# Performance work log

Measured on AMD Instinct MI355X. Metric: run time of the kernel, lower is better.

The kernel has to match this reference:

```python
import jax, jax.numpy as jnp
import numpy as np

B, S, H, D = 4, 2048, 16, 64


def setup_inputs() -> dict:
    key = jax.random.key(0)
    kq, kk, kv, kl = jax.random.split(key, 4)
    qs = jax.random.normal(kq, (B, S, H, D), dtype=jnp.float32)
    ks = jax.random.normal(kk, (B, S, H, D), dtype=jnp.float32)
    vs = jax.random.normal(kv, (B, S, H, D), dtype=jnp.float32)
    # valid lengths in [S//2, S] so no sequence is fully masked out
    valid_lens = jax.random.randint(kl, (B,), S // 2, S + 1, dtype=jnp.int32)
    return {"qs": qs, "ks": ks, "vs": vs, "valid_lens": valid_lens}


def reference(qs, ks, vs, valid_lens):
    # ScanAttention == exact softmax attention (FlashAttention-2 is an
    # IO-aware reformulation of the same math). qs scaled by 1/sqrt(D).
    d = qs.shape[-1]
    scale = 1.0 / jnp.sqrt(jnp.asarray(d, qs.dtype))
    # scores: [B, H, Q, K]
    scores = jnp.einsum('bqhd,bkhd->bhqk', qs * scale, ks)
    # key mask from valid_lens: position k is valid iff k < valid_lens[b]
    k_len = ks.shape[1]
    ks_mask = jnp.arange(k_len)[None, :] < valid_lens[:, None]  # [B, K]
    scores = jnp.where(ks_mask[:, None, None, :], scores, -jnp.inf)
    attn = jax.nn.softmax(scores, axis=-1)
    ctx = jnp.einsum('bhqk,bkhd->bqhd', attn, vs)
    return ctx
```

## Files before the change

### kernel.cpp

```cpp
#include <hip/hip_runtime.h>
#include <hip/hip_bf16.h>

typedef __bf16 bf16x8 __attribute__((ext_vector_type(8)));
typedef float  f32x4  __attribute__((ext_vector_type(4)));
typedef float  f32x16 __attribute__((ext_vector_type(16)));
typedef float  f4     __attribute__((ext_vector_type(4)));
typedef unsigned int u32;
typedef u32 u32x4 __attribute__((ext_vector_type(4)));

#define MFMA16(a,b,c) __builtin_amdgcn_mfma_f32_16x16x32_bf16(a,b,c,0,0,0)
#define MFMA32(a,b,c) __builtin_amdgcn_mfma_f32_32x32x16_bf16(a,b,c,0,0,0)

constexpr int   Bc = 4, Sc = 2048, Hc = 16, Dc = 64;
constexpr int   HD  = Hc * Dc;
constexpr int   SHD = Sc * HD;
constexpr float SCALE = 0.125f;
constexpr float LOG2E = 1.4426950408889634f;
constexpr float QSC   = SCALE * LOG2E;
constexpr float NEG   = -1e30f;
constexpr int   HEAD_ELEMS = Sc * Dc;
constexpr size_t KV_ELEMS  = (size_t)Bc * Hc * HEAD_ELEMS;

__global__ __launch_bounds__(256) void prep2(
    const float* __restrict__ K, const float* __restrict__ V,
    __bf16* __restrict__ Kf, __bf16* __restrict__ Vf)
{
    __shared__ __align__(16) __bf16 KT[64][80];
    __shared__ __align__(16) __bf16 VT[64][80];

    const int bid = blockIdx.x;
    const int st  = bid & 31;
    const int h   = (bid >> 5) & 15;
    const int b   = bid >> 9;
    const int tid = threadIdx.x;
    const int sl  = tid >> 2;
    const int d0  = (tid & 3) * 16;
    const size_t iof = ((size_t)(b * 2048 + st * 64 + sl) * 16 + h) * 64 + d0;

    #pragma unroll
    for (int q = 0; q < 2; ++q) {
        f4 a = __builtin_nontemporal_load((const f4*)(K + iof + q * 8));
        f4 c = __builtin_nontemporal_load((const f4*)(K + iof + q * 8 + 4));
        bf16x8 w;
        w[0]=(__bf16)a.x; w[1]=(__bf16)a.y; w[2]=(__bf16)a.z; w[3]=(__bf16)a.w;
        w[4]=(__bf16)c.x; w[5]=(__bf16)c.y; w[6]=(__bf16)c.z; w[7]=(__bf16)c.w;
        *(bf16x8*)&KT[sl][d0 + q * 8] = w;
    }
    #pragma unroll
    for (int q = 0; q < 2; ++q) {
        f4 a = __builtin_nontemporal_load((const f4*)(V + iof + q * 8));
        f4 c = __builtin_nontemporal_load((const f4*)(V + iof + q * 8 + 4));
        bf16x8 w;
        w[0]=(__bf16)a.x; w[1]=(__bf16)a.y; w[2]=(__bf16)a.z; w[3]=(__bf16)a.w;
        w[4]=(__bf16)c.x; w[5]=(__bf16)c.y; w[6]=(__bf16)c.z; w[7]=(__bf16)c.w;
        *(bf16x8*)&VT[sl][d0 + q * 8] = w;
    }
    __syncthreads();

    const size_t hbase = (size_t)(b * 16 + h) * HEAD_ELEMS;

    #pragma unroll
    for (int it = 0; it < 2; ++it) {
        const int idx = it * 256 + tid;
        const int tl  = idx >> 8;
        const int dk  = (idx >> 6) & 3;
        const int ln  = idx & 63;
        const int l31 = ln & 31, lhi = ln >> 5;
        bf16x8 w = *(const bf16x8*)&KT[tl * 32 + l31][dk * 16 + lhi * 8];
        *(bf16x8*)(Kf + hbase + (size_t)(((st * 2 + tl) * 4 + dk) * 512 + ln * 8)) = w;
    }
    #pragma unroll
    for (int it = 0; it < 2; ++it) {
        const int idx  = it * 256 + tid;
        const int tl   = idx >> 8;
        const int dblk = (idx >> 7) & 1;
        const int kt2  = (idx >> 6) & 1;
        const int ln   = idx & 63;
        const int l31  = ln & 31, lhi = ln >> 5;
        bf16x8 w;
        #pragma unroll
        for (int j = 0; j < 8; ++j)
            w[j] = VT[tl * 32 + kt2 * 16 + lhi * 8 + j][dblk * 32 + l31];
        *(bf16x8*)(Vf + hbase +
            (size_t)(((((st * 2 + tl) * 2 + dblk) * 2 + kt2)) * 512 + ln * 8)) = w;
    }
}

__global__ __launch_bounds__(64, 4) void fattn4(
    const float* __restrict__ Q, const __bf16* __restrict__ Kf,
    const __bf16* __restrict__ Vf, const int* __restrict__ VL,
    float* __restrict__ O)
{
    const int bid  = blockIdx.x;
    const int l    = (bid & 7) * 512 + (bid >> 3);
    const int head = l >> 6;
    const int qt   = l & 63;
    const int b    = head >> 4;
    const int h    = head & 15;
    const int lane = threadIdx.x;
    const int l31  = lane & 31;
    const int hi   = lane >> 5;
    const int vl   = VL[b];

    const size_t qbase = (size_t)b * SHD + (size_t)h * Dc;
    const __bf16* kfh = Kf + (size_t)head * HEAD_ELEMS + lane * 8;
    const __bf16* vfh = Vf + (size_t)head * HEAD_ELEMS + lane * 8;
    const int qrow0 = qt * 32;

    bf16x8 qf[4];
    {
        const float* qp = Q + qbase + (size_t)(qrow0 + l31) * HD + hi * 8;
        #pragma unroll
        for (int dk = 0; dk < 4; ++dk) {
            f4 x0 = __builtin_nontemporal_load((const f4*)(qp + dk * 16));
            f4 x1 = __builtin_nontemporal_load((const f4*)(qp + dk * 16 + 4));
            bf16x8 f;
            f[0]=(__bf16)(x0.x*QSC); f[1]=(__bf16)(x0.y*QSC);
            f[2]=(__bf16)(x0.z*QSC); f[3]=(__bf16)(x0.w*QSC);
            f[4]=(__bf16)(x1.x*QSC); f[5]=(__bf16)(x1.y*QSC);
            f[6]=(__bf16)(x1.z*QSC); f[7]=(__bf16)(x1.w*QSC);
            qf[dk] = f;
        }
    }

    f32x16 acc0, acc1;
    #pragma unroll
    for (int i = 0; i < 16; ++i) { acc0[i] = 0.f; acc1[i] = 0.f; }
    float m = NEG, lsum = 0.f;

    const int nt   = (vl + 31) >> 5;
    const int ntm1 = nt - 1;
    const bool hastail = (vl & 31) != 0;

    bf16x8 kf[4], vf[4];
    #pragma unroll
    for (int dk = 0; dk < 4; ++dk) kf[dk] = *(const bf16x8*)(kfh + dk * 512);
    #pragma unroll
    for (int i = 0; i < 4; ++i)   vf[i]  = *(const bf16x8*)(vfh + i * 512);

    for (int t = 0; t < nt; ++t) {
        f32x16 s;
        #pragma unroll
        for (int i = 0; i < 16; ++i) s[i] = 0.f;
        #pragma unroll
        for (int dk = 0; dk < 4; ++dk) s = MFMA32(kf[dk], qf[dk], s);

        {
            const size_t off = (size_t)((t < ntm1) ? t + 1 : t) * 2048;
            #pragma unroll
            for (int dk = 0; dk < 4; ++dk)
                kf[dk] = *(const bf16x8*)(kfh + off + dk * 512);
        }

        if (t == ntm1 && hastail) {
            const int kv0 = t * 32;
            #pragma unroll
            for (int i = 0; i < 16; ++i) {
                const int key = kv0 + (i & 3) + 8 * (i >> 2) + 4 * hi;
                if (key >= vl) s[i] = NEG;
            }
        }

        float a0 = fmaxf(s[0], s[1]),  a1 = fmaxf(s[2], s[3]);
        float a2 = fmaxf(s[4], s[5]),  a3 = fmaxf(s[6], s[7]);
        float a4 = fmaxf(s[8], s[9]),  a5 = fmaxf(s[10], s[11]);
        float a6 = fmaxf(s[12], s[13]), a7 = fmaxf(s[14], s[15]);
        float b0 = fmaxf(a0, a1), b1 = fmaxf(a2, a3);
        float b2 = fmaxf(a4, a5), b3 = fmaxf(a6, a7);
        float tm = fmaxf(fmaxf(b0, b1), fmaxf(b2, b3));
        tm = fmaxf(tm, __shfl_xor(tm, 32));

        if (__any(tm > m + 8.0f)) {
            const float mn  = fmaxf(m, tm);
            const float fac = __builtin_amdgcn_exp2f(m - mn);
            lsum *= fac;
            #pragma unroll
            for (int i = 0; i < 16; ++i) { acc0[i] *= fac; acc1[i] *= fac; }
            m = mn;
        }
        #pragma unroll
        for (int i = 0; i < 16; ++i)
            s[i] = __builtin_amdgcn_exp2f(s[i] - m);
        {
            float t0 = (s[0]+s[1]) + (s[2]+s[3]);
            float t1 = (s[4]+s[5]) + (s[6]+s[7]);
            float t2 = (s[8]+s[9]) + (s[10]+s[11]);
            float t3 = (s[12]+s[13]) + (s[14]+s[15]);
            lsum += (t0 + t1) + (t2 + t3);
        }

        bf16x8 ap[2];
        #pragma unroll
        for (int kt = 0; kt < 2; ++kt) {
            u32 w0, w1, w2, w3;
            asm("v_cvt_pk_bf16_f32 %0, %1, %2" : "=v"(w0) : "v"(s[8*kt+0]), "v"(s[8*kt+1]));
            asm("v_cvt_pk_bf16_f32 %0, %1, %2" : "=v"(w1) : "v"(s[8*kt+2]), "v"(s[8*kt+3]));
            asm("v_cvt_pk_bf16_f32 %0, %1, %2" : "=v"(w2) : "v"(s[8*kt+4]), "v"(s[8*kt+5]));
            asm("v_cvt_pk_bf16_f32 %0, %1, %2" : "=v"(w3) : "v"(s[8*kt+6]), "v"(s[8*kt+7]));
            const u32 sx0 = (u32)__shfl_xor((int)w0, 32);
            const u32 sx1 = (u32)__shfl_xor((int)w1, 32);
            const u32 sx2 = (u32)__shfl_xor((int)w2, 32);
            const u32 sx3 = (u32)__shfl_xor((int)w3, 32);
            u32x4 fw;
            fw.x = hi ? sx2 : w0;
            fw.y = hi ? sx3 : w1;
            fw.z = hi ? w2 : sx0;
            fw.w = hi ? w3 : sx1;
            ap[kt] = __builtin_bit_cast(bf16x8, fw);
        }

        acc0 = MFMA32(vf[0], ap[0], acc0);
        acc0 = MFMA32(vf[1], ap[1], acc0);
        acc1 = MFMA32(vf[2], ap[0], acc1);
        acc1 = MFMA32(vf[3], ap[1], acc1);

        {
            const size_t off = (size_t)((t < ntm1) ? t + 1 : t) * 2048;
            #pragma unroll
            for (int i = 0; i < 4; ++i)
                vf[i] = *(const bf16x8*)(vfh + off + i * 512);
        }
    }

    const float lfull = lsum + __shfl_xor(lsum, 32);
    const float linv  = 1.0f / lfull;
    float* op = O + qbase + (size_t)(qrow0 + l31) * HD;
    #pragma unroll
    for (int qd = 0; qd < 4; ++qd) {
        f4 w0, w1;
        w0.x = acc0[4*qd+0]*linv; w0.y = acc0[4*qd+1]*linv;
        w0.z = acc0[4*qd+2]*linv; w0.w = acc0[4*qd+3]*linv;
        w1.x = acc1[4*qd+0]*linv; w1.y = acc1[4*qd+1]*linv;
        w1.z = acc1[4*qd+2]*linv; w1.w = acc1[4*qd+3]*linv;
        __builtin_nontemporal_store(w0, (f4*)(op + qd * 8 + 4 * hi));
        __builtin_nontemporal_store(w1, (f4*)(op + 32 + qd * 8 + 4 * hi));
    }
}

__global__ __launch_bounds__(256, 2) void fattn_fb(
    const float* __restrict__ Q, const float* __restrict__ K,
    const float* __restrict__ V, const int* __restrict__ VL,
    float* __restrict__ O)
{
    __shared__ __bf16 Vts[64 * 64];
    __shared__ __bf16 Pl[4][32 * 64];
    const int bid = blockIdx.x;
    const int qt = bid & 15, h = (bid >> 4) & 15, b = bid >> 8;
    const int tid = threadIdx.x, wid = tid >> 6, lane = tid & 63;
    const int li = lane & 15, lg = lane >> 4;
    const int vl = VL[b];
    const size_t base = (size_t)b * SHD + (size_t)h * Dc;
    bf16x8 aq[2][2];
    const int qrow0 = qt * 128 + wid * 32;
    #pragma unroll
    for (int m = 0; m < 2; ++m) {
        const float* qp = Q + base + (size_t)(qrow0 + m * 16 + li) * HD + lg * 8;
        #pragma unroll
        for (int ks = 0; ks < 2; ++ks) {
            float4 x0 = *(const float4*)(qp + ks * 32);
            float4 x1 = *(const float4*)(qp + ks * 32 + 4);
            bf16x8 f;
            f[0]=(__bf16)(x0.x*QSC); f[1]=(__bf16)(x0.y*QSC);
            f[2]=(__bf16)(x0.z*QSC); f[3]=(__bf16)(x0.w*QSC);
            f[4]=(__bf16)(x1.x*QSC); f[5]=(__bf16)(x1.y*QSC);
            f[6]=(__bf16)(x1.z*QSC); f[7]=(__bf16)(x1.w*QSC);
            aq[m][ks] = f;
        }
    }
    bf16x8 bones;
    #pragma unroll
    for (int j = 0; j < 8; ++j) bones[j] = (__bf16)1.0f;
    f32x4 acc[2][4]; float mst[2][4], lst[2][4];
    #pragma unroll
    for (int m = 0; m < 2; ++m) {
        #pragma unroll
        for (int r = 0; r < 4; ++r) { mst[m][r] = NEG; lst[m][r] = 0.f; }
        #pragma unroll
        for (int dt = 0; dt < 4; ++dt)
            #pragma unroll
            for (int r = 0; r < 4; ++r) acc[m][dt][r] = 0.f;
    }
    const int ntiles = (vl + 63) >> 6;
    const int sd = tid & 63, skb = (tid >> 6) * 8;
    const float* vpd = V + base + sd;
    for (int t = 0; t < ntiles; ++t) {
        const int kv0 = t * 64;
        __syncthreads();
        #pragma unroll
        for (int rep = 0; rep < 2; ++rep) {
            const int kb2 = skb + rep * 32;
            bf16x8 pk;
            #pragma unroll
            for (int j = 0; j < 8; ++j) pk[j] = (__bf16)vpd[(size_t)(kv0+kb2+j)*HD];
            *(bf16x8*)&Vts[(sd*64+kb2) ^ ((sd&7)<<3)] = pk;
        }
        __syncthreads();
        f32x4 s[2][4];
        #pragma unroll
        for (int m = 0; m < 2; ++m)
            #pragma unroll
            for (int nt2 = 0; nt2 < 4; ++nt2)
                #pragma unroll
                for (int r = 0; r < 4; ++r) s[m][nt2][r] = 0.f;
        #pragma unroll
        for (int nt2 = 0; nt2 < 4; ++nt2) {
            const float* kp = K + base + (size_t)(kv0+nt2*16+li)*HD + lg*8;
            #pragma unroll
            for (int ks = 0; ks < 2; ++ks) {
                float4 x0 = *(const float4*)(kp + ks*32);
                float4 x1 = *(const float4*)(kp + ks*32 + 4);
                bf16x8 f;
                f[0]=(__bf16)x0.x; f[1]=(__bf16)x0.y; f[2]=(__bf16)x0.z; f[3]=(__bf16)x0.w;
                f[4]=(__bf16)x1.x; f[5]=(__bf16)x1.y; f[6]=(__bf16)x1.z; f[7]=(__bf16)x1.w;
                #pragma unroll
                for (int m = 0; m < 2; ++m) s[m][nt2] = MFMA16(aq[m][ks], f, s[m][nt2]);
            }
        }
        bool kva[4];
        #pragma unroll
        for (int nt2 = 0; nt2 < 4; ++nt2) kva[nt2] = (kv0 + nt2*16 + li) < vl;
        #pragma unroll
        for (int m = 0; m < 2; ++m)
            #pragma unroll
            for (int nt2 = 0; nt2 < 4; ++nt2)
                #pragma unroll
                for (int r = 0; r < 4; ++r)
                    if (!kva[nt2]) s[m][nt2][r] = NEG;
        #pragma unroll
        for (int m = 0; m < 2; ++m) {
            #pragma unroll
            for (int r = 0; r < 4; ++r) {
                float tmx = fmaxf(fmaxf(s[m][0][r], s[m][1][r]),
                                  fmaxf(s[m][2][r], s[m][3][r]));
                tmx = fmaxf(tmx, __shfl_xor(tmx, 1));
                tmx = fmaxf(tmx, __shfl_xor(tmx, 2));
                tmx = fmaxf(tmx, __shfl_xor(tmx, 4));
                tmx = fmaxf(tmx, __shfl_xor(tmx, 8));
                const float mn = fmaxf(mst[m][r], tmx);
                const float fac = __builtin_amdgcn_exp2f(mst[m][r] - mn);
                mst[m][r] = mn; lst[m][r] *= fac;
                #pragma unroll
                for (int dt = 0; dt < 4; ++dt) acc[m][dt][r] *= fac;
                const int qr = m*16 + lg*4 + r, swz = (qr & 7) << 3;
                #pragma unroll
                for (int nt2 = 0; nt2 < 4; ++nt2)
                    Pl[wid][(qr*64 + nt2*16 + li) ^ swz] =
                        (__bf16)__builtin_amdgcn_exp2f(s[m][nt2][r] - mn);
            }
        }
        bf16x8 ap[2][2];
        #pragma unroll
        for (int m = 0; m < 2; ++m) {
            const int qr = m*16 + li, swz = (qr & 7) << 3;
            #pragma unroll
            for (int ks = 0; ks < 2; ++ks)
                ap[m][ks] = *(bf16x8*)&Pl[wid][(qr*64 + ks*32 + lg*8) ^ swz];
        }
        #pragma unroll
        for (int m = 0; m < 2; ++m) {
            f32x4 rs;
            #pragma unroll
            for (int r = 0; r < 4; ++r) rs[r] = 0.f;
            rs = MFMA16(ap[m][0], bones, rs);
            rs = MFMA16(ap[m][1], bones, rs);
            #pragma unroll
            for (int r = 0; r < 4; ++r) lst[m][r] += rs[r];
        }
        #pragma unroll
        for (int dt = 0; dt < 4; ++dt) {
            const int d = dt*16 + li, swz = (d & 7) << 3;
            #pragma unroll
            for (int ks = 0; ks < 2; ++ks) {
                bf16x8 bv = *(bf16x8*)&Vts[(d*64 + ks*32 + lg*8) ^ swz];
                #pragma unroll
                for (int m = 0; m < 2; ++m)
                    acc[m][dt] = MFMA16(ap[m][ks], bv, acc[m][dt]);
            }
        }
    }
    #pragma unroll
    for (int m = 0; m < 2; ++m) {
        #pragma unroll
        for (int r = 0; r < 4; ++r) {
            const float inv = 1.0f / lst[m][r];
            float* op = O + base + (size_t)(qrow0 + m*16 + lg*4 + r) * HD;
            #pragma unroll
            for (int dt = 0; dt < 4; ++dt) op[dt*16 + li] = acc[m][dt][r] * inv;
        }
    }
}

extern "C" void kernel_launch(void* const* d_in, const int* in_sizes, int n_in,
                              void* d_out, int out_size, void* d_ws, size_t ws_size,
                              hipStream_t stream) {
    (void)in_sizes; (void)n_in; (void)out_size;
    const float* q    = (const float*)d_in[0];
    const float* k    = (const float*)d_in[1];
    const float* v    = (const float*)d_in[2];
    const int*   vlen = (const int*)d_in[3];
    float*       out  = (float*)d_out;
    const size_t need = 2 * KV_ELEMS * sizeof(__bf16);
    if (ws_size >= need) {
        __bf16* kfp = (__bf16*)d_ws;
        __bf16* vfp = kfp + KV_ELEMS;
        prep2<<<dim3(2048), 256, 0, stream>>>(k, v, kfp, vfp);
        fattn4<<<dim3(4096), 64, 0, stream>>>(q, kfp, vfp, vlen, out);
    } else {
        fattn_fb<<<dim3(1024), 256, 0, stream>>>(q, k, v, vlen, out);
    }
}
```

Before: 124.9 us.

## Remap blocks to XCDs, use permlane32 swap, max3 reduction, plain stores

Changes the block-to-(head, q-tile) mapping so each XCD processes a set of heads interleaved across q-tiles, which alters L2 locality of the K/V reads. It replaces four cross-half shuffles plus selects with two v_permlane32_swap instructions when building the P operand. It restructures the row-max reduction into fmax3-friendly groupings and changes the nontemporal output stores to regular stores. Several unrelated micro-optimizations are bundled, and the new mapping changes which blocks share K/V in each XCD's L2.

```diff
diff --git a/kernel.cpp b/kernel.cpp
--- a/kernel.cpp
+++ b/kernel.cpp
@@ -92,9 +92,10 @@
     float* __restrict__ O)
 {
     const int bid  = blockIdx.x;
-    const int l    = (bid & 7) * 512 + (bid >> 3);
-    const int head = l >> 6;
-    const int qt   = l & 63;
+    const int xcd  = bid & 7;
+    const int idx  = bid >> 3;
+    const int head = xcd + (idx & 7) * 8;
+    const int qt   = idx >> 3;
     const int b    = head >> 4;
     const int h    = head & 15;
     const int lane = threadIdx.x;
@@ -161,13 +162,14 @@
             }
         }
 
-        float a0 = fmaxf(s[0], s[1]),  a1 = fmaxf(s[2], s[3]);
-        float a2 = fmaxf(s[4], s[5]),  a3 = fmaxf(s[6], s[7]);
-        float a4 = fmaxf(s[8], s[9]),  a5 = fmaxf(s[10], s[11]);
-        float a6 = fmaxf(s[12], s[13]), a7 = fmaxf(s[14], s[15]);
-        float b0 = fmaxf(a0, a1), b1 = fmaxf(a2, a3);
-        float b2 = fmaxf(a4, a5), b3 = fmaxf(a6, a7);
-        float tm = fmaxf(fmaxf(b0, b1), fmaxf(b2, b3));
+        float c0 = fmaxf(fmaxf(s[0],  s[1]),  s[2]);
+        float c1 = fmaxf(fmaxf(s[3],  s[4]),  s[5]);
+        float c2 = fmaxf(fmaxf(s[6],  s[7]),  s[8]);
+        float c3 = fmaxf(fmaxf(s[9],  s[10]), s[11]);
+        float c4 = fmaxf(fmaxf(s[12], s[13]), s[14]);
+        float c5 = fmaxf(fmaxf(c0, c1), s[15]);
+        float c6 = fmaxf(fmaxf(c2, c3), c4);
+        float tm = fmaxf(c5, c6);
         tm = fmaxf(tm, __shfl_xor(tm, 32));
 
         if (__any(tm > m + 8.0f)) {
@@ -197,15 +199,13 @@
             asm("v_cvt_pk_bf16_f32 %0, %1, %2" : "=v"(w1) : "v"(s[8*kt+2]), "v"(s[8*kt+3]));
             asm("v_cvt_pk_bf16_f32 %0, %1, %2" : "=v"(w2) : "v"(s[8*kt+4]), "v"(s[8*kt+5]));
             asm("v_cvt_pk_bf16_f32 %0, %1, %2" : "=v"(w3) : "v"(s[8*kt+6]), "v"(s[8*kt+7]));
-            const u32 sx0 = (u32)__shfl_xor((int)w0, 32);
-            const u32 sx1 = (u32)__shfl_xor((int)w1, 32);
-            const u32 sx2 = (u32)__shfl_xor((int)w2, 32);
-            const u32 sx3 = (u32)__shfl_xor((int)w3, 32);
+            asm("v_permlane32_swap_b32 %0, %1" : "+v"(w0), "+v"(w2));
+            asm("v_permlane32_swap_b32 %0, %1" : "+v"(w1), "+v"(w3));
             u32x4 fw;
-            fw.x = hi ? sx2 : w0;
-            fw.y = hi ? sx3 : w1;
-            fw.z = hi ? w2 : sx0;
-            fw.w = hi ? w3 : sx1;
+            fw.x = w0;
+            fw.y = w1;
+            fw.z = w2;
+            fw.w = w3;
             ap[kt] = __builtin_bit_cast(bf16x8, fw);
         }
 
@@ -232,8 +232,8 @@
         w0.z = acc0[4*qd+2]*linv; w0.w = acc0[4*qd+3]*linv;
         w1.x = acc1[4*qd+0]*linv; w1.y = acc1[4*qd+1]*linv;
         w1.z = acc1[4*qd+2]*linv; w1.w = acc1[4*qd+3]*linv;
-        __builtin_nontemporal_store(w0, (f4*)(op + qd * 8 + 4 * hi));
-        __builtin_nontemporal_store(w1, (f4*)(op + 32 + qd * 8 + 4 * hi));
+        *(f4*)(op + qd * 8 + 4 * hi)      = w0;
+        *(f4*)(op + 32 + qd * 8 + 4 * hi) = w1;
     }
 }
 
```

After: 117.6 us. -5.8%, faster.
